# Kernel optimization log

Hardware: AMD Instinct MI355X
Metric: run time of the kernel (lower is better)

## Reference

```python
import jax, jax.numpy as jnp
import numpy as np

N = 50000      # nodes
E = 800000     # edges
D_IN = 300     # input node feature dim
D_H = 96       # hidden dim
D_OUT = 2      # classes
G = 64         # graphs in batch


def setup_inputs() -> dict:
    key = jax.random.key(0)
    ks = jax.random.split(key, 10)
    x = jax.random.normal(ks[0], (N, D_IN), dtype=jnp.float32)
    src = jax.random.randint(ks[1], (E,), 0, N, dtype=jnp.int32)
    dst = jax.random.randint(ks[2], (E,), 0, N, dtype=jnp.int32)
    batch = jnp.sort(jax.random.randint(ks[3], (N,), 0, G, dtype=jnp.int32))
    # GCNConv: linear weight (no bias in lin), separate additive bias (PyG default)
    W1 = jax.random.normal(ks[4], (D_IN, D_H), jnp.float32) / np.sqrt(D_IN)
    b1 = jnp.zeros((D_H,), jnp.float32)
    W2 = jax.random.normal(ks[5], (D_H, D_H), jnp.float32) / np.sqrt(D_H)
    b2 = jnp.zeros((D_H,), jnp.float32)
    Wfc = jax.random.normal(ks[6], (D_H, D_OUT), jnp.float32) / np.sqrt(D_H)
    bfc = jnp.zeros((D_OUT,), jnp.float32)
    return {"x": x, "W1": W1, "b1": b1, "W2": W2, "b2": b2,
            "Wfc": Wfc, "bfc": bfc, "src": src, "dst": dst, "batch": batch}


def _gcn_conv(h_in, W, b, src, dst, deg_inv_sqrt):
    """PyG GCNConv with self-loops: out = D^-1/2 (A+I) D^-1/2 (h W) + b."""
    h = h_in @ W                                   # [N, F] transform first
    norm = deg_inv_sqrt[src] * deg_inv_sqrt[dst]   # [E]
    msg = h[src] * norm[:, None]                   # gather + scale (dominant traffic)
    agg = jax.ops.segment_sum(msg, dst, num_segments=N)
    agg = agg + h * (deg_inv_sqrt * deg_inv_sqrt)[:, None]  # self-loop term
    return agg + b


def reference(x, W1, b1, W2, b2, Wfc, bfc, src, dst, batch):
    # degree with self loops, computed on destination nodes (PyG convention)
    deg = jax.ops.segment_sum(jnp.ones((E,), x.dtype), dst, num_segments=N) + 1.0
    dis = jax.lax.rsqrt(deg)
    h = jax.nn.relu(_gcn_conv(x, W1, b1, src, dst, dis))   # dropout = identity (eval)
    h = jax.nn.relu(_gcn_conv(h, W2, b2, src, dst, dis))
    # global mean pool over per-graph node segments
    counts = jax.ops.segment_sum(jnp.ones((N,), x.dtype), batch, num_segments=G)
    pooled = jax.ops.segment_sum(h, batch, num_segments=G) / jnp.maximum(counts, 1.0)[:, None]
    return pooled @ Wfc + bfc                               # [G, D_OUT]
```

## Files before the change

### kernel.cpp

```cpp
#include <hip/hip_runtime.h>
#include <hip/hip_bf16.h>

#define NN 50000
#define NE 800000
#define DIN 300
#define KP1 320
#define DH 96
#define DOUTC 2
#define NG 64

#define NKB 10
#define NFRAG (NKB * 6 * 64)

#define DSTRIDE 64
#define NB1 ((NN + 63) / 64)
#define EPB 1024
#define NB2 ((NN + 31) / 32)
#define LROW 104

typedef __attribute__((ext_vector_type(8))) short bf16x8;
typedef __attribute__((ext_vector_type(4))) float f32x4;

__device__ inline unsigned short f2bf(float f) {
    unsigned int u = __float_as_uint(f);
    unsigned int r = (u + 0x7fffu + ((u >> 16) & 1u)) >> 16;
    return (unsigned short)r;
}
__device__ inline float b2f(unsigned short u) {
    return __uint_as_float((unsigned int)u << 16);
}

__global__ void k_prep(int* cnt, float* pooled,
                       const float* __restrict__ W1, unsigned short* __restrict__ wt1f,
                       const float* __restrict__ W2, unsigned short* __restrict__ wt2) {
    int i = blockIdx.x * blockDim.x + threadIdx.x;
    if (i < NN) cnt[i] = 0;
    if (i < NG * DH) pooled[i] = 0.f;
    if (i < NFRAG * 8) {
        int j = i & 7;
        int f = i >> 3;
        int lane = f & 63;
        int ft = f >> 6;
        int t = ft % 6;
        int kb = ft / 6;
        int row = (lane & 15) + 16 * t;
        int col = kb * 32 + (lane >> 4) * 8 + j;
        wt1f[i] = (col < DIN) ? f2bf(W1[(size_t)col * DH + row]) : (unsigned short)0;
    }
    if (i < DH * DH) {
        int j = i / DH, k = i - j * DH;
        wt2[i] = f2bf(W2[(size_t)k * DH + j]);
    }
}

__global__ __launch_bounds__(256) void k_g1sc(const float* __restrict__ A,
        const unsigned short* __restrict__ WF, unsigned short* __restrict__ Cb,
        const int* __restrict__ src, const int* __restrict__ dst,
        int* cnt, unsigned short* __restrict__ esrc) {
    __shared__ unsigned short ldsB[NFRAG * 8];
    const int tid = threadIdx.x;

    if (blockIdx.x & 1) {
        const int ebase = (blockIdx.x >> 1) * EPB + tid * 4;
        if (ebase + 3 < NE) {
            int4 d4 = *(const int4*)&dst[ebase];
            int4 s4 = *(const int4*)&src[ebase];
            int p0 = atomicAdd(&cnt[d4.x], 1);
            int p1 = atomicAdd(&cnt[d4.y], 1);
            int p2 = atomicAdd(&cnt[d4.z], 1);
            int p3 = atomicAdd(&cnt[d4.w], 1);
            if (p0 < DSTRIDE) esrc[(size_t)d4.x * DSTRIDE + p0] = (unsigned short)s4.x;
            if (p1 < DSTRIDE) esrc[(size_t)d4.y * DSTRIDE + p1] = (unsigned short)s4.y;
            if (p2 < DSTRIDE) esrc[(size_t)d4.z * DSTRIDE + p2] = (unsigned short)s4.z;
            if (p3 < DSTRIDE) esrc[(size_t)d4.w * DSTRIDE + p3] = (unsigned short)s4.w;
        } else {
            for (int e = ebase; e < NE; ++e) {
                int d = dst[e];
                int pos = atomicAdd(&cnt[d], 1);
                if (pos < DSTRIDE) esrc[(size_t)d * DSTRIDE + pos] = (unsigned short)src[e];
            }
        }
        return;
    }

    const int tile = blockIdx.x >> 1;
    {
        const uint4* srcv = (const uint4*)WF;
        uint4* dstv = (uint4*)ldsB;
        #pragma unroll
        for (int f = 0; f < NFRAG / 256; ++f)
            dstv[f * 256 + tid] = srcv[f * 256 + tid];
    }
    __syncthreads();

    const int wv = tid >> 6;
    const int lane = tid & 63;
    const int m = lane & 15;
    const int quad = lane >> 4;
    const int row = tile * 64 + wv * 16 + m;
    const int arow = row < NN ? row : NN - 1;
    const float* ap = A + (size_t)arow * DIN + quad * 8;
    const float4 z4 = make_float4(0.f, 0.f, 0.f, 0.f);
    const bf16x8* lb = (const bf16x8*)ldsB;
    f32x4 acc[6];
    #pragma unroll
    for (int t = 0; t < 6; ++t) acc[t] = (f32x4){0.f, 0.f, 0.f, 0.f};

    float4 pa[4][2];
    #pragma unroll
    for (int i = 0; i < 3; ++i) {
        int kb = i * 32 + quad * 8;
        pa[i][0] = (kb + 4 <= DIN) ? *(const float4*)(ap + i * 32) : z4;
        pa[i][1] = (kb + 8 <= DIN) ? *(const float4*)(ap + i * 32 + 4) : z4;
    }

    #pragma unroll
    for (int i = 0; i < NKB; ++i) {
        if (i + 3 < NKB) {
            int kb = (i + 3) * 32 + quad * 8;
            pa[(i + 3) & 3][0] = (kb + 4 <= DIN) ? *(const float4*)(ap + (i + 3) * 32) : z4;
            pa[(i + 3) & 3][1] = (kb + 8 <= DIN) ? *(const float4*)(ap + (i + 3) * 32 + 4) : z4;
        }
        float4 a0 = pa[i & 3][0], a1 = pa[i & 3][1];
        bf16x8 af;
        af[0] = (short)f2bf(a0.x); af[1] = (short)f2bf(a0.y);
        af[2] = (short)f2bf(a0.z); af[3] = (short)f2bf(a0.w);
        af[4] = (short)f2bf(a1.x); af[5] = (short)f2bf(a1.y);
        af[6] = (short)f2bf(a1.z); af[7] = (short)f2bf(a1.w);
        #pragma unroll
        for (int t = 0; t < 6; ++t) {
            bf16x8 bf = lb[(i * 6 + t) * 64 + lane];
            acc[t] = __builtin_amdgcn_mfma_f32_16x16x32_bf16(af, bf, acc[t], 0, 0, 0);
        }
    }
    const int rbase = tile * 64 + wv * 16 + quad * 4;
    #pragma unroll
    for (int r = 0; r < 4; ++r) {
        int rr = rbase + r;
        if (rr < NN) {
            unsigned short* cp = Cb + (size_t)rr * DH + m;
            #pragma unroll
            for (int t = 0; t < 6; ++t) cp[t * 16] = f2bf(acc[t][r]);
        }
    }
}

__global__ __launch_bounds__(128) void k_agg1g2(const ushort4* __restrict__ hb,
        const int* __restrict__ cnt, const unsigned short* __restrict__ esrc,
        const float4* __restrict__ bias4, const unsigned short* __restrict__ WT,
        unsigned short* __restrict__ Cb) {
    __shared__ unsigned short a1l[32 * LROW];
    const int tid = threadIdx.x;
    const int n0 = blockIdx.x * 32;

    #pragma unroll
    for (int it = 0; it < 6; ++it) {
        int item = tid + it * 128;
        int nl = item / 24;
        int q = item - nl * 24;
        int n = n0 + nl;
        ushort4 o = make_ushort4(0, 0, 0, 0);
        if (n < NN) {
            int count = cnt[n];
            float dn = rsqrtf(1.0f + (float)count);
            if (count > DSTRIDE) count = DSTRIDE;
            const int beg = n * DSTRIDE;
            const int end = beg + count;
            ushort4 u0 = hb[(size_t)n * 24 + q];
            float4 acc = make_float4(dn * b2f(u0.x), dn * b2f(u0.y),
                                     dn * b2f(u0.z), dn * b2f(u0.w));
            int e = beg;
            for (; e + 3 < end; e += 4) {
                int s0 = esrc[e], s1 = esrc[e + 1], s2 = esrc[e + 2], s3 = esrc[e + 3];
                float d0 = rsqrtf(1.0f + (float)cnt[s0]);
                float d1 = rsqrtf(1.0f + (float)cnt[s1]);
                float d2 = rsqrtf(1.0f + (float)cnt[s2]);
                float d3 = rsqrtf(1.0f + (float)cnt[s3]);
                ushort4 v0 = hb[(size_t)s0 * 24 + q];
                ushort4 v1 = hb[(size_t)s1 * 24 + q];
                ushort4 v2 = hb[(size_t)s2 * 24 + q];
                ushort4 v3 = hb[(size_t)s3 * 24 + q];
                acc.x = fmaf(d0, b2f(v0.x), acc.x); acc.y = fmaf(d0, b2f(v0.y), acc.y);
                acc.z = fmaf(d0, b2f(v0.z), acc.z); acc.w = fmaf(d0, b2f(v0.w), acc.w);
                acc.x = fmaf(d1, b2f(v1.x), acc.x); acc.y = fmaf(d1, b2f(v1.y), acc.y);
                acc.z = fmaf(d1, b2f(v1.z), acc.z); acc.w = fmaf(d1, b2f(v1.w), acc.w);
                acc.x = fmaf(d2, b2f(v2.x), acc.x); acc.y = fmaf(d2, b2f(v2.y), acc.y);
                acc.z = fmaf(d2, b2f(v2.z), acc.z); acc.w = fmaf(d2, b2f(v2.w), acc.w);
                acc.x = fmaf(d3, b2f(v3.x), acc.x); acc.y = fmaf(d3, b2f(v3.y), acc.y);
                acc.z = fmaf(d3, b2f(v3.z), acc.z); acc.w = fmaf(d3, b2f(v3.w), acc.w);
            }
            for (; e < end; ++e) {
                int s = esrc[e];
                float ds = rsqrtf(1.0f + (float)cnt[s]);
                ushort4 v = hb[(size_t)s * 24 + q];
                acc.x = fmaf(ds, b2f(v.x), acc.x);
                acc.y = fmaf(ds, b2f(v.y), acc.y);
                acc.z = fmaf(ds, b2f(v.z), acc.z);
                acc.w = fmaf(ds, b2f(v.w), acc.w);
            }
            float4 b = bias4[q];
            o.x = f2bf(fmaxf(fmaf(dn, acc.x, b.x), 0.f));
            o.y = f2bf(fmaxf(fmaf(dn, acc.y, b.y), 0.f));
            o.z = f2bf(fmaxf(fmaf(dn, acc.z, b.z), 0.f));
            o.w = f2bf(fmaxf(fmaf(dn, acc.w, b.w), 0.f));
        }
        *(ushort4*)&a1l[nl * LROW + q * 4] = o;
    }
    __syncthreads();

    const int wv = tid >> 6;
    const int lane = tid & 63;
    const int m = lane & 15;
    const int quad = lane >> 4;
    const unsigned short* ap = &a1l[(wv * 16 + m) * LROW + quad * 8];
    const unsigned short* wp = WT + (size_t)m * DH + quad * 8;
    bf16x8 af[3], bf[3][6];
    #pragma unroll
    for (int i = 0; i < 3; ++i) af[i] = *(const bf16x8*)(ap + i * 32);
    #pragma unroll
    for (int i = 0; i < 3; ++i)
        #pragma unroll
        for (int t = 0; t < 6; ++t)
            bf[i][t] = *(const bf16x8*)(wp + (size_t)t * 16 * DH + i * 32);
    f32x4 acc[6];
    #pragma unroll
    for (int t = 0; t < 6; ++t) acc[t] = (f32x4){0.f, 0.f, 0.f, 0.f};
    #pragma unroll
    for (int i = 0; i < 3; ++i)
        #pragma unroll
        for (int t = 0; t < 6; ++t)
            acc[t] = __builtin_amdgcn_mfma_f32_16x16x32_bf16(af[i], bf[i][t], acc[t], 0, 0, 0);
    const int rbase = n0 + wv * 16 + quad * 4;
    #pragma unroll
    for (int r = 0; r < 4; ++r) {
        int rr = rbase + r;
        if (rr < NN) {
            unsigned short* cp = Cb + (size_t)rr * DH + m;
            #pragma unroll
            for (int t = 0; t < 6; ++t) cp[t * 16] = f2bf(acc[t][r]);
        }
    }
}

#define QH (DH / 4)
__global__ void k_agg2(const ushort4* __restrict__ hb,
                       const int* __restrict__ cnt,
                       const unsigned short* __restrict__ esrc,
                       const float4* __restrict__ bias4, float4* __restrict__ fout) {
    int gid = blockIdx.x * blockDim.x + threadIdx.x;
    if (gid >= NN * QH) return;
    int n = gid / QH;
    int q = gid - n * QH;
    int count = cnt[n];
    float dn = rsqrtf(1.0f + (float)count);
    if (count > DSTRIDE) count = DSTRIDE;
    const int beg = n * DSTRIDE;
    const int end = beg + count;
    ushort4 u0 = hb[(size_t)n * QH + q];
    float4 acc = make_float4(dn * b2f(u0.x), dn * b2f(u0.y), dn * b2f(u0.z), dn * b2f(u0.w));
    int e = beg;
    for (; e + 3 < end; e += 4) {
        int s0 = esrc[e], s1 = esrc[e + 1], s2 = esrc[e + 2], s3 = esrc[e + 3];
        float d0 = rsqrtf(1.0f + (float)cnt[s0]);
        float d1 = rsqrtf(1.0f + (float)cnt[s1]);
        float d2 = rsqrtf(1.0f + (float)cnt[s2]);
        float d3 = rsqrtf(1.0f + (float)cnt[s3]);
        ushort4 v0 = hb[(size_t)s0 * QH + q];
        ushort4 v1 = hb[(size_t)s1 * QH + q];
        ushort4 v2 = hb[(size_t)s2 * QH + q];
        ushort4 v3 = hb[(size_t)s3 * QH + q];
        acc.x = fmaf(d0, b2f(v0.x), acc.x); acc.y = fmaf(d0, b2f(v0.y), acc.y);
        acc.z = fmaf(d0, b2f(v0.z), acc.z); acc.w = fmaf(d0, b2f(v0.w), acc.w);
        acc.x = fmaf(d1, b2f(v1.x), acc.x); acc.y = fmaf(d1, b2f(v1.y), acc.y);
        acc.z = fmaf(d1, b2f(v1.z), acc.z); acc.w = fmaf(d1, b2f(v1.w), acc.w);
        acc.x = fmaf(d2, b2f(v2.x), acc.x); acc.y = fmaf(d2, b2f(v2.y), acc.y);
        acc.z = fmaf(d2, b2f(v2.z), acc.z); acc.w = fmaf(d2, b2f(v2.w), acc.w);
        acc.x = fmaf(d3, b2f(v3.x), acc.x); acc.y = fmaf(d3, b2f(v3.y), acc.y);
        acc.z = fmaf(d3, b2f(v3.z), acc.z); acc.w = fmaf(d3, b2f(v3.w), acc.w);
    }
    for (; e < end; ++e) {
        int s = esrc[e];
        float ds = rsqrtf(1.0f + (float)cnt[s]);
        ushort4 v = hb[(size_t)s * QH + q];
        acc.x = fmaf(ds, b2f(v.x), acc.x);
        acc.y = fmaf(ds, b2f(v.y), acc.y);
        acc.z = fmaf(ds, b2f(v.z), acc.z);
        acc.w = fmaf(ds, b2f(v.w), acc.w);
    }
    float4 b = bias4[q];
    float4 r;
    r.x = fmaxf(fmaf(dn, acc.x, b.x), 0.f);
    r.y = fmaxf(fmaf(dn, acc.y, b.y), 0.f);
    r.z = fmaxf(fmaf(dn, acc.z, b.z), 0.f);
    r.w = fmaxf(fmaf(dn, acc.w, b.w), 0.f);
    fout[gid] = r;
}

#define PNODES 32
__global__ void k_pool_partial(const float* __restrict__ h, const int* __restrict__ batch,
                               float* __restrict__ pooled) {
    __shared__ int sbatch[PNODES];
    const int n0 = blockIdx.x * PNODES;
    const int nend = min(n0 + PNODES, NN);
    const int cnt = nend - n0;
    const int f = threadIdx.x;
    if (f < cnt) sbatch[f] = batch[n0 + f];
    __syncthreads();
    if (f < DH) {
        float acc = 0.f;
        int cur = sbatch[0];
        for (int i = 0; i < cnt; ++i) {
            int g = sbatch[i];
            if (g != cur) {
                atomicAdd(&pooled[cur * DH + f], acc);
                acc = 0.f; cur = g;
            }
            acc += h[(size_t)(n0 + i) * DH + f];
        }
        atomicAdd(&pooled[cur * DH + f], acc);
    }
}

__global__ void k_fc(const float* __restrict__ pooled, const int* __restrict__ batch,
                     const float* __restrict__ Wfc, const float* __restrict__ bfc,
                     float* __restrict__ out) {
    const int t = threadIdx.x;
    if (t >= NG * DOUTC) return;
    const int g = t / DOUTC;
    const int c = t - g * DOUTC;
    int lo = 0, hi = NN;
    while (lo < hi) { int mid = (lo + hi) >> 1; if (batch[mid] < g) lo = mid + 1; else hi = mid; }
    const int s = lo;
    hi = NN;
    while (lo < hi) { int mid = (lo + hi) >> 1; if (batch[mid] < g + 1) lo = mid + 1; else hi = mid; }
    float inv = 1.f / fmaxf((float)(lo - s), 1.f);
    float acc = bfc[c];
    #pragma unroll 8
    for (int j = 0; j < DH; ++j)
        acc += pooled[g * DH + j] * inv * Wfc[j * DOUTC + c];
    out[g * DOUTC + c] = acc;
}

extern "C" void kernel_launch(void* const* d_in, const int* in_sizes, int n_in,
                              void* d_out, int out_size, void* d_ws, size_t ws_size,
                              hipStream_t stream) {
    const float* x   = (const float*)d_in[0];
    const float* W1  = (const float*)d_in[1];
    const float* b1  = (const float*)d_in[2];
    const float* W2  = (const float*)d_in[3];
    const float* b2  = (const float*)d_in[4];
    const float* Wfc = (const float*)d_in[5];
    const float* bfc = (const float*)d_in[6];
    const int* src   = (const int*)d_in[7];
    const int* dst   = (const int*)d_in[8];
    const int* batch = (const int*)d_in[9];
    float* out = (float*)d_out;

    unsigned short* hb  = (unsigned short*)d_ws;
    float* hbuf  = (float*)(hb + (size_t)NN * DH);
    float* pooled= hbuf + (size_t)NN * DH;
    int* cnt     = (int*)(pooled + NG * DH);
    unsigned short* esrc = (unsigned short*)(cnt + NN);
    unsigned short* wt1f = esrc + (size_t)NN * DSTRIDE;
    unsigned short* wt2  = wt1f + NFRAG * 8;

    const int TB = 256;
    k_prep<<<(NN + TB - 1) / TB, TB, 0, stream>>>(cnt, pooled, W1, wt1f, W2, wt2);
    k_g1sc<<<NB1 * 2, 256, 0, stream>>>(x, wt1f, hb, src, dst, cnt, esrc);
    k_agg1g2<<<NB2, 128, 0, stream>>>((const ushort4*)hb, cnt, esrc,
                                      (const float4*)b1, wt2, hb);
    k_agg2<<<(NN * QH + TB - 1) / TB, TB, 0, stream>>>(
        (const ushort4*)hb, cnt, esrc, (const float4*)b2, (float4*)hbuf);
    k_pool_partial<<<(NN + PNODES - 1) / PNODES, 128, 0, stream>>>(hbuf, batch, pooled);
    k_fc<<<1, 128, 0, stream>>>(pooled, batch, Wfc, bfc, out);
}
```

Before: 249.1 us.

## Use one thread per node-quad in agg1 gather and separate output buffer

The fused layer-1 aggregation plus layer-2 GEMM kernel now launches 768 threads per block so each thread handles one (node, feature-quad) item instead of looping six times. This exposes more memory-level parallelism for the neighbor gathers. Only the first two waves run the MFMA stage, which now loops over output tiles to reduce register pressure. The GEMM output is written to a new buffer instead of in place over the gather source, which removes a read/write hazard between blocks.

Result: no change. 246.9 us (-0.9%).

```diff
diff --git a/kernel.cpp b/kernel.cpp
--- a/kernel.cpp
+++ b/kernel.cpp
@@ -145,7 +145,7 @@
     }
 }
 
-__global__ __launch_bounds__(128) void k_agg1g2(const ushort4* __restrict__ hb,
+__global__ __launch_bounds__(768) void k_agg1g2(const ushort4* __restrict__ hb,
         const int* __restrict__ cnt, const unsigned short* __restrict__ esrc,
         const float4* __restrict__ bias4, const unsigned short* __restrict__ WT,
         unsigned short* __restrict__ Cb) {
@@ -153,11 +153,9 @@
     const int tid = threadIdx.x;
     const int n0 = blockIdx.x * 32;
 
-    #pragma unroll
-    for (int it = 0; it < 6; ++it) {
-        int item = tid + it * 128;
-        int nl = item / 24;
-        int q = item - nl * 24;
+    {
+        int nl = tid / 24;
+        int q = tid - nl * 24;
         int n = n0 + nl;
         ushort4 o = make_ushort4(0, 0, 0, 0);
         if (n < NN) {
@@ -208,36 +206,30 @@
     }
     __syncthreads();
 
-    const int wv = tid >> 6;
-    const int lane = tid & 63;
-    const int m = lane & 15;
-    const int quad = lane >> 4;
-    const unsigned short* ap = &a1l[(wv * 16 + m) * LROW + quad * 8];
-    const unsigned short* wp = WT + (size_t)m * DH + quad * 8;
-    bf16x8 af[3], bf[3][6];
-    #pragma unroll
-    for (int i = 0; i < 3; ++i) af[i] = *(const bf16x8*)(ap + i * 32);
-    #pragma unroll
-    for (int i = 0; i < 3; ++i)
+    if (tid < 128) {
+        const int wv = tid >> 6;
+        const int lane = tid & 63;
+        const int m = lane & 15;
+        const int quad = lane >> 4;
+        const unsigned short* ap = &a1l[(wv * 16 + m) * LROW + quad * 8];
+        const unsigned short* wp = WT + (size_t)m * DH + quad * 8;
+        bf16x8 af[3];
         #pragma unroll
-        for (int t = 0; t < 6; ++t)
-            bf[i][t] = *(const bf16x8*)(wp + (size_t)t * 16 * DH + i * 32);
-    f32x4 acc[6];
-    #pragma unroll
-    for (int t = 0; t < 6; ++t) acc[t] = (f32x4){0.f, 0.f, 0.f, 0.f};
-    #pragma unroll
-    for (int i = 0; i < 3; ++i)
-        #pragma unroll
-        for (int t = 0; t < 6; ++t)
-            acc[t] = __builtin_amdgcn_mfma_f32_16x16x32_bf16(af[i], bf[i][t], acc[t], 0, 0, 0);
-    const int rbase = n0 + wv * 16 + quad * 4;
-    #pragma unroll
-    for (int r = 0; r < 4; ++r) {
-        int rr = rbase + r;
-        if (rr < NN) {
-            unsigned short* cp = Cb + (size_t)rr * DH + m;
+        for (int i = 0; i < 3; ++i) af[i] = *(const bf16x8*)(ap + i * 32);
+        const int rbase = n0 + wv * 16 + quad * 4;
+        #pragma unroll 1
+        for (int t = 0; t < 6; ++t) {
+            f32x4 acc = (f32x4){0.f, 0.f, 0.f, 0.f};
             #pragma unroll
-            for (int t = 0; t < 6; ++t) cp[t * 16] = f2bf(acc[t][r]);
+            for (int i = 0; i < 3; ++i) {
+                bf16x8 bf = *(const bf16x8*)(wp + (size_t)t * 16 * DH + i * 32);
+                acc = __builtin_amdgcn_mfma_f32_16x16x32_bf16(af[i], bf, acc, 0, 0, 0);
+            }
+            #pragma unroll
+            for (int r = 0; r < 4; ++r) {
+                int rr = rbase + r;
+                if (rr < NN) Cb[(size_t)rr * DH + m + t * 16] = f2bf(acc[r]);
+            }
         }
     }
 }
@@ -357,7 +349,8 @@
     float* out = (float*)d_out;
 
     unsigned short* hb  = (unsigned short*)d_ws;
-    float* hbuf  = (float*)(hb + (size_t)NN * DH);
+    unsigned short* h2b = hb + (size_t)NN * DH;
+    float* hbuf  = (float*)(h2b + (size_t)NN * DH);
     float* pooled= hbuf + (size_t)NN * DH;
     int* cnt     = (int*)(pooled + NG * DH);
     unsigned short* esrc = (unsigned short*)(cnt + NN);
@@ -367,10 +360,10 @@
     const int TB = 256;
     k_prep<<<(NN + TB - 1) / TB, TB, 0, stream>>>(cnt, pooled, W1, wt1f, W2, wt2);
     k_g1sc<<<NB1 * 2, 256, 0, stream>>>(x, wt1f, hb, src, dst, cnt, esrc);
-    k_agg1g2<<<NB2, 128, 0, stream>>>((const ushort4*)hb, cnt, esrc,
-                                      (const float4*)b1, wt2, hb);
+    k_agg1g2<<<NB2, 768, 0, stream>>>((const ushort4*)hb, cnt, esrc,
+                                      (const float4*)b1, wt2, h2b);
     k_agg2<<<(NN * QH + TB - 1) / TB, TB, 0, stream>>>(
-        (const ushort4*)hb, cnt, esrc, (const float4*)b2, (float4*)hbuf);
+        (const ushort4*)h2b, cnt, esrc, (const float4*)b2, (float4*)hbuf);
     k_pool_partial<<<(NN + PNODES - 1) / PNODES, 128, 0, stream>>>(hbuf, batch, pooled);
     k_fc<<<1, 128, 0, stream>>>(pooled, batch, Wfc, bfc, out);
 }
```
